# Performance work log

Hardware: AMD Instinct MI355X
Metric: run time of the kernel (lower is better)

Reference implementation:

```python
import jax, jax.numpy as jnp
import numpy as np
import math

# ---- hyperparameters (init_kwargs) ----
D = 2              # spatial dimension
MTOT = 65          # quadrature nodes per dimension (odd)
LENGTHSCALE = 0.1  # SE kernel lengthscale
OUTPUTSCALE = 1.0  # SE kernel variance
SIGMASQ = 0.05     # observation noise variance
CG_ITERS = 30      # fixed CG iteration count (replaces tol-based early stopping)
N_TRAIN = 100000
N_TEST = 50000
TWO_PI = 2.0 * math.pi


def setup_inputs() -> dict:
    key = jax.random.key(0)
    k1, k2, k3 = jax.random.split(key, 3)
    x = jax.random.uniform(k1, (N_TRAIN, D), dtype=jnp.float32)
    y = jax.random.normal(k2, (N_TRAIN,), dtype=jnp.float32)
    x_new = jax.random.uniform(k3, (N_TEST, D), dtype=jnp.float32)
    return {"x": x, "y": y, "x_new": x_new}


def _phases(col, h, freqs, isign):
    # exp(isign * i * 2*pi*h * x * k), shape [N, K]
    return jnp.exp((1j * isign * TWO_PI) * (h * col[:, None] * freqs[None, :]).astype(jnp.float32))


def _nudft_type1(pts, c, h, freqs):
    # fk[a,b] = sum_n c_n exp(-2*pi*i*h*(k_a x_n0 + k_b x_n1)); separable tensor grid
    E0 = _phases(pts[:, 0], h, freqs, -1.0)
    E1 = _phases(pts[:, 1], h, freqs, -1.0)
    return jnp.einsum('n,na,nb->ab', c.astype(jnp.complex64), E0, E1)


def _nudft_type2(pts, fk, h, freqs):
    # f_n = sum_{a,b} fk[a,b] exp(+2*pi*i*h*(k_a x_n0 + k_b x_n1))
    E0 = _phases(pts[:, 0], h, freqs, +1.0)
    E1 = _phases(pts[:, 1], h, freqs, +1.0)
    return jnp.einsum('ab,na,nb->n', fk, E0, E1)


def _cg(A, b, iters):
    # complex Hermitian-PSD conjugate gradients, fixed iteration count
    x0 = jnp.zeros_like(b)
    r0 = b
    rs0 = jnp.real(jnp.vdot(r0, r0))

    def step(carry, _):
        xk, r, p, rs = carry
        Ap = A(p)
        alpha = rs / jnp.real(jnp.vdot(p, Ap))
        xk = xk + alpha * p
        r = r - alpha * Ap
        rs_new = jnp.real(jnp.vdot(r, r))
        p = r + (rs_new / rs) * p
        return (xk, r, p, rs_new), None

    (xk, _, _, _), _ = jax.lax.scan(step, (x0, r0, r0, rs0), None, length=iters)
    return xk


def _forward(x, y, x_new):
    m = (MTOT - 1) // 2
    # geometry / quadrature (get_xis): domain extent L, spacing h = 1/L, grid k = -m..m
    x_all = jnp.concatenate((x, x_new), axis=0)
    L = jnp.max(jnp.max(x_all, axis=0) - jnp.min(x_all, axis=0))
    L = jnp.where(L <= 1e-9, jnp.float32(1.0), L)
    h = (1.0 / L).astype(jnp.float32)
    k = (jnp.arange(MTOT) - m).astype(jnp.float32)
    xis_1d = h * k
    X0, X1 = jnp.meshgrid(xis_1d, xis_1d, indexing='ij')
    sq = X0 * X0 + X1 * X1  # [MTOT, MTOT] squared frequency norm
    # squared-exponential spectral density S(s) = sigma_f^2 (2*pi*l^2)^(d/2) exp(-2*pi^2*l^2 |s|^2)
    l2 = LENGTHSCALE * LENGTHSCALE
    spec = OUTPUTSCALE * (TWO_PI * l2) ** (D / 2) * jnp.exp((-2.0 * math.pi ** 2 * l2) * sq)
    ws = jnp.sqrt(spec * h ** D).reshape(-1).astype(jnp.complex64)  # [M]

    # rhs = ws * F^H y  (type-1 NUFFT, exact NUDFT)
    rhs = ws * _nudft_type1(x, y, h, k).reshape(-1)

    # Toeplitz convolution vector v[o] = sum_n exp(-2*pi*i*h*o.x_n), offsets -(mtot-1)..(mtot-1)
    kk = (jnp.arange(2 * MTOT - 1) - (MTOT - 1)).astype(jnp.float32)
    Ev0 = _phases(x[:, 0], h, kk, -1.0)
    Ev1 = _phases(x[:, 1], h, kk, -1.0)
    v = jnp.einsum('na,nb->ab', Ev0, Ev1)  # [2M-1, 2M-1]
    # circularly align offset 0 to index 0, precompute FFT
    v_circ = jnp.roll(v, shift=(-(MTOT - 1), -(MTOT - 1)), axis=(0, 1))
    vhat = jnp.fft.fftn(v_circ)
    s_fft = (2 * MTOT - 1, 2 * MTOT - 1)

    def toeplitz_apply(w):  # w: [MTOT, MTOT] complex
        W = jnp.fft.fftn(w, s=s_fft)
        full = jnp.fft.ifftn(vhat * W)
        return full[:MTOT, :MTOT]

    def A_mean(beta):  # (W F^H F W + sigma^2 I) beta, beta flat [M]
        wb = (ws * beta).reshape(MTOT, MTOT)
        Tw = toeplitz_apply(wb).reshape(-1)
        return ws * Tw + SIGMASQ * beta

    beta = _cg(A_mean, rhs, CG_ITERS)
    # posterior mean at test points via type-2 NUFFT
    yhat = jnp.real(_nudft_type2(x_new, (ws * beta).reshape(MTOT, MTOT), h, k))
    return yhat


def reference(x, y, x_new):
    return _forward(x, y, x_new)
```

## Files before the change

kernel.cpp:

```cpp
#include <hip/hip_runtime.h>
#include <math.h>

#define M2 4225
#define NTRAIN 100000
#define NTEST 50000
#define CGITERS 30
#define TWO_PI_D 6.283185307179586476925287
#define TPI32 6.28318530717958647692f

#define F_H 0
#define F_RS 1
#define F_PAP 2
#define F_RSN 3
#define F_WS 8
#define F_RHS 4234
#define F_X 12684
#define F_R 21134
#define F_P 29584
#define F_AP 38034
#define F_PB 46484
#define F_VF 50710
#define F_VHAT 83992
#define F_PROD 117274
#define D_VPART 125330
#define D_FKPART 2271890

#define NCHUNK 128
#define PTSB2 782
#define VHALF 8385
#define VH2 16770
#define FKHALF 2145
#define FH2 4290

__device__ __forceinline__ unsigned fkey(float f){
  unsigned u = __float_as_uint(f);
  return (u & 0x80000000u) ? ~u : (u | 0x80000000u);
}
__device__ __forceinline__ float fdec(unsigned k){
  unsigned u = (k & 0x80000000u) ? (k & 0x7fffffffu) : ~k;
  return __uint_as_float(u);
}

__global__ void k_init(unsigned* mm){
  if (threadIdx.x == 0){
    mm[0] = 0xFFFFFFFFu; mm[1] = 0u; mm[2] = 0xFFFFFFFFu; mm[3] = 0u;
  }
}

__global__ void k_minmax(const float* __restrict__ x, const float* __restrict__ xn,
                         unsigned* __restrict__ mm){
  int tid = blockIdx.x * blockDim.x + threadIdx.x;
  int str = gridDim.x * blockDim.x;
  float mn0 = 1e30f, mx0 = -1e30f, mn1 = 1e30f, mx1 = -1e30f;
  const float2* a = (const float2*)x;
  for (int i = tid; i < NTRAIN; i += str){
    float2 v = a[i];
    mn0 = fminf(mn0, v.x); mx0 = fmaxf(mx0, v.x);
    mn1 = fminf(mn1, v.y); mx1 = fmaxf(mx1, v.y);
  }
  const float2* b = (const float2*)xn;
  for (int i = tid; i < NTEST; i += str){
    float2 v = b[i];
    mn0 = fminf(mn0, v.x); mx0 = fmaxf(mx0, v.x);
    mn1 = fminf(mn1, v.y); mx1 = fmaxf(mx1, v.y);
  }
  for (int off = 32; off; off >>= 1){
    mn0 = fminf(mn0, __shfl_xor(mn0, off, 64));
    mx0 = fmaxf(mx0, __shfl_xor(mx0, off, 64));
    mn1 = fminf(mn1, __shfl_xor(mn1, off, 64));
    mx1 = fmaxf(mx1, __shfl_xor(mx1, off, 64));
  }
  if ((threadIdx.x & 63) == 0){
    atomicMin(&mm[0], fkey(mn0)); atomicMax(&mm[1], fkey(mx0));
    atomicMin(&mm[2], fkey(mn1)); atomicMax(&mm[3], fkey(mx1));
  }
}

__global__ void k_setup(float* __restrict__ wsf){
  const unsigned* mm = (const unsigned*)(wsf + 4);
  float mn0 = fdec(mm[0]), mx0 = fdec(mm[1]);
  float mn1 = fdec(mm[2]), mx1 = fdec(mm[3]);
  float d0 = __fsub_rn(mx0, mn0), d1 = __fsub_rn(mx1, mn1);
  float L = fmaxf(d0, d1);
  if (L <= 1e-9f) L = 1.0f;
  float hf = __fdiv_rn(1.0f, L);
  if (threadIdx.x == 0) wsf[F_H] = hf;
  const float c0f = (float)(TWO_PI_D * 0.01);
  const float c1f = (float)(-2.0 * 9.869604401089358618834 * 0.01);
  float h2f = __fmul_rn(hf, hf);
  for (int e = threadIdx.x; e < M2; e += blockDim.x){
    int r = e / 65, c = e - r * 65;
    float xi0 = __fmul_rn(hf, (float)(r - 32));
    float xi1 = __fmul_rn(hf, (float)(c - 32));
    float sq = __fadd_rn(__fmul_rn(xi0, xi0), __fmul_rn(xi1, xi1));
    float spec = __fmul_rn(c0f, expf(__fmul_rn(c1f, sq)));
    wsf[F_WS + e] = sqrtf(__fmul_rn(spec, h2f));
  }
}

__launch_bounds__(256)
__global__ void k_v_main(const float* __restrict__ x, const float* __restrict__ wsf,
                         double* __restrict__ vpart){
  __shared__ float2 aL[16][80];
  __shared__ float2 bL[16][16];
  __shared__ float hxs[16][2];
  const float hf = wsf[F_H];
  const int tid = threadIdx.x;
  const int t0 = tid >> 4, t1 = tid & 15;
  const int jcol = blockIdx.y * 16 + t1;
  double2 acc[5];
  #pragma unroll
  for (int k = 0; k < 5; ++k) acc[k] = make_double2(0.0, 0.0);
  const int p0 = blockIdx.x * PTSB2;
  const int pend = min(p0 + PTSB2, NTRAIN);
  for (int base = p0; base < pend; base += 16){
    if (tid < 32){
      int p = tid >> 1, d = tid & 1;
      int gp = base + p;
      hxs[p][d] = (gp < pend) ? __fmul_rn(hf, x[2 * gp + d]) : 0.f;
    }
    __syncthreads();
    for (int i = tid; i < 16 * 80; i += 256){
      int p = i / 80;
      int o = i - p * 80;
      int gp = base + p;
      float2 va = make_float2(0.f, 0.f);
      if (gp < pend && o < 65){
        float t = __fmul_rn(hxs[p][0], (float)o);
        float sn, cs; sincosf(__fmul_rn(TPI32, t), &sn, &cs);
        va = make_float2(cs, -sn);
      }
      aL[p][o] = va;
    }
    {
      int p = t0, c = t1;
      int gp = base + p;
      int j = blockIdx.y * 16 + c;
      float2 vb = make_float2(0.f, 0.f);
      if (gp < pend && j < 129){
        float t = __fmul_rn(hxs[p][1], (float)(j - 64));
        float sn, cs; sincosf(__fmul_rn(TPI32, t), &sn, &cs);
        vb = make_float2(cs, -sn);
      }
      bL[p][c] = vb;
    }
    __syncthreads();
    #pragma unroll 1
    for (int p = 0; p < 16; ++p){
      float2 bv = bL[p][t1];
      float2 av[5];
      #pragma unroll
      for (int k = 0; k < 5; ++k) av[k] = aL[p][t0 + 16 * k];
      #pragma unroll
      for (int k = 0; k < 5; ++k){
        acc[k].x += (double)av[k].x * (double)bv.x - (double)av[k].y * (double)bv.y;
        acc[k].y += (double)av[k].x * (double)bv.y + (double)av[k].y * (double)bv.x;
      }
    }
    __syncthreads();
  }
  double* outp = vpart + (size_t)blockIdx.x * VH2;
  if (jcol < 129){
    #pragma unroll
    for (int k = 0; k < 5; ++k){
      int o0 = t0 + 16 * k;
      if (o0 < 65){
        int e = o0 * 129 + jcol;
        outp[2 * e] = acc[k].x;
        outp[2 * e + 1] = acc[k].y;
      }
    }
  }
}

__launch_bounds__(256)
__global__ void k_fk_main(const float* __restrict__ x, const float* __restrict__ y,
                          const float* __restrict__ wsf, double* __restrict__ fkpart){
  __shared__ float2 aL[16][48];
  __shared__ float2 bL[16][16];
  __shared__ float hxs[16][2];
  __shared__ float ys[16];
  const float hf = wsf[F_H];
  const int tid = threadIdx.x;
  const int t0 = tid >> 4, t1 = tid & 15;
  const int jcol = blockIdx.y * 16 + t1;
  double2 acc[3];
  #pragma unroll
  for (int k = 0; k < 3; ++k) acc[k] = make_double2(0.0, 0.0);
  const int p0 = blockIdx.x * PTSB2;
  const int pend = min(p0 + PTSB2, NTRAIN);
  for (int base = p0; base < pend; base += 16){
    if (tid < 32){
      int p = tid >> 1, d = tid & 1;
      int gp = base + p;
      hxs[p][d] = (gp < pend) ? __fmul_rn(hf, x[2 * gp + d]) : 0.f;
    } else if (tid < 48){
      int p = tid - 32;
      int gp = base + p;
      ys[p] = (gp < pend) ? y[gp] : 0.f;
    }
    __syncthreads();
    for (int i = tid; i < 16 * 48; i += 256){
      int p = i / 48, o = i - p * 48;
      int gp = base + p;
      float2 val = make_float2(0.f, 0.f);
      if (o < 33 && gp < pend){
        float t = __fmul_rn(hxs[p][0], (float)o);
        float sn, cs; sincosf(__fmul_rn(TPI32, t), &sn, &cs);
        val = make_float2(__fmul_rn(ys[p], cs), __fmul_rn(ys[p], -sn));
      }
      aL[p][o] = val;
    }
    {
      int p = t0, c = t1;
      int gp = base + p;
      int j = blockIdx.y * 16 + c;
      float2 vb = make_float2(0.f, 0.f);
      if (gp < pend && j < 65){
        float t = __fmul_rn(hxs[p][1], (float)(j - 32));
        float sn, cs; sincosf(__fmul_rn(TPI32, t), &sn, &cs);
        vb = make_float2(cs, -sn);
      }
      bL[p][c] = vb;
    }
    __syncthreads();
    #pragma unroll 1
    for (int p = 0; p < 16; ++p){
      float2 bv = bL[p][t1];
      float2 av[3];
      #pragma unroll
      for (int k = 0; k < 3; ++k) av[k] = aL[p][t0 + 16 * k];
      #pragma unroll
      for (int k = 0; k < 3; ++k){
        acc[k].x += (double)av[k].x * (double)bv.x - (double)av[k].y * (double)bv.y;
        acc[k].y += (double)av[k].x * (double)bv.y + (double)av[k].y * (double)bv.x;
      }
    }
    __syncthreads();
  }
  double* outp = fkpart + (size_t)blockIdx.x * FH2;
  if (jcol < 65){
    #pragma unroll
    for (int k = 0; k < 3; ++k){
      int o0 = t0 + 16 * k;
      if (o0 < 33){
        int e = o0 * 65 + jcol;
        outp[2 * e] = acc[k].x;
        outp[2 * e + 1] = acc[k].y;
      }
    }
  }
}

__global__ void k_reduce_v(const double* __restrict__ wsd, float* __restrict__ wsf){
  int e = blockIdx.x * blockDim.x + threadIdx.x;
  if (e >= VHALF) return;
  const double* vp = wsd + D_VPART;
  double sr = 0.0, si = 0.0;
  for (int k = 0; k < NCHUNK; ++k){
    sr += vp[(size_t)k * VH2 + 2 * e];
    si += vp[(size_t)k * VH2 + 2 * e + 1];
  }
  float r32 = (float)sr, i32 = (float)si;
  int o0 = e / 129, j = e - o0 * 129;
  float2* vF = (float2*)(wsf + F_VF);
  vF[(o0 + 64) * 129 + j] = make_float2(r32, i32);
  if (o0 > 0) vF[(64 - o0) * 129 + (128 - j)] = make_float2(r32, -i32);
}

__global__ void k_reduce_fk(const double* __restrict__ wsd, float* __restrict__ wsf){
  int e = blockIdx.x * blockDim.x + threadIdx.x;
  if (e >= FKHALF) return;
  const double* fp = wsd + D_FKPART;
  double sr = 0.0, si = 0.0;
  for (int k = 0; k < NCHUNK; ++k){
    sr += fp[(size_t)k * FH2 + 2 * e];
    si += fp[(size_t)k * FH2 + 2 * e + 1];
  }
  float fr = (float)sr, fi = (float)si;
  int a = e / 65, c = e - a * 65;
  int ef = (a + 32) * 65 + c;
  float wf = wsf[F_WS + ef];
  float* rhs = wsf + F_RHS;
  rhs[2 * ef] = __fmul_rn(wf, fr);
  rhs[2 * ef + 1] = __fmul_rn(wf, fi);
  if (a > 0){
    int ef2 = (32 - a) * 65 + (64 - c);
    float wf2 = wsf[F_WS + ef2];
    rhs[2 * ef2] = __fmul_rn(wf2, fr);
    rhs[2 * ef2 + 1] = -__fmul_rn(wf2, fi);
  }
}

__launch_bounds__(192)
__global__ void k_vhat(float* __restrict__ wsf){
  __shared__ double twc[129], tws[129];
  __shared__ double t1r[129], t1i[129];
  int p = blockIdx.x, t = threadIdx.x;
  if (t < 129){
    double ang = TWO_PI_D * (double)t / 129.0;
    double s, c; sincos(ang, &s, &c);
    twc[t] = c; tws[t] = s;
  }
  __syncthreads();
  if (t < 129){
    const float2* vF = (const float2*)(wsf + F_VF);
    int n = t;
    int nsrc = (n + 64) % 129;
    double ar = 0.0, ai = 0.0;
    for (int m = 0; m < 129; ++m){
      float2 v = vF[((m + 64) % 129) * 129 + nsrc];
      int idx = (p * m) % 129;
      double wr = twc[idx], wi = -tws[idx];
      ar += (double)v.x * wr - (double)v.y * wi;
      ai += (double)v.x * wi + (double)v.y * wr;
    }
    t1r[n] = ar; t1i[n] = ai;
  }
  __syncthreads();
  if (t < 129){
    int q = t;
    double ar = 0.0, ai = 0.0;
    for (int n = 0; n < 129; ++n){
      int idx = (q * n) % 129;
      double wr = twc[idx], wi = -tws[idx];
      ar += t1r[n] * wr - t1i[n] * wi;
      ai += t1r[n] * wi + t1i[n] * wr;
    }
    ((float2*)(wsf + F_VHAT))[p * 129 + q] = make_float2((float)ar, (float)ai);
  }
}

__global__ void k_cg_init(float* __restrict__ wsf){
  int e = blockIdx.x * blockDim.x + threadIdx.x;
  if (e >= M2) return;
  const float2* rhs = (const float2*)(wsf + F_RHS);
  float2 b = rhs[e];
  ((float2*)(wsf + F_X))[e] = make_float2(0.f, 0.f);
  ((float2*)(wsf + F_R))[e] = b;
  ((float2*)(wsf + F_P))[e] = b;
  wsf[F_PB + e] = __fadd_rn(__fmul_rn(b.x, b.x), __fmul_rn(b.y, b.y));
}

__device__ __forceinline__ float pw_leaf(const float* d, int o, int n){
  float r0 = d[o], r1 = d[o+1], r2 = d[o+2], r3 = d[o+3];
  float r4 = d[o+4], r5 = d[o+5], r6 = d[o+6], r7 = d[o+7];
  int i = 8;
  int lim = n - (n & 7);
  for (; i < lim; i += 8){
    r0 = __fadd_rn(r0, d[o+i]);   r1 = __fadd_rn(r1, d[o+i+1]);
    r2 = __fadd_rn(r2, d[o+i+2]); r3 = __fadd_rn(r3, d[o+i+3]);
    r4 = __fadd_rn(r4, d[o+i+4]); r5 = __fadd_rn(r5, d[o+i+5]);
    r6 = __fadd_rn(r6, d[o+i+6]); r7 = __fadd_rn(r7, d[o+i+7]);
  }
  float res = __fadd_rn(__fadd_rn(__fadd_rn(r0, r1), __fadd_rn(r2, r3)),
                        __fadd_rn(__fadd_rn(r4, r5), __fadd_rn(r6, r7)));
  for (; i < n; ++i) res = __fadd_rn(res, d[o+i]);
  return res;
}

__device__ __forceinline__ void pw_tree(const float* pb, float* T, int tid){
  if (tid < 16){
    const int tb[16] = {0,264,528,792,1056,1320,1584,1848,
                        2112,2376,2640,2904,3168,3432,3696,3960};
    int base = tb[tid];
    int sz3 = (tid == 15) ? 73 : 72;
    float L0 = pw_leaf(pb, base, 128);
    float L1 = pw_leaf(pb, base + 128, 64);
    float L2 = pw_leaf(pb, base + 192, sz3);
    T[tid] = __fadd_rn(L0, __fadd_rn(L1, L2));
  }
  __syncthreads();
  if (tid == 0){
    float s0 = __fadd_rn(__fadd_rn(T[0], T[1]), __fadd_rn(T[2], T[3]));
    float s1 = __fadd_rn(__fadd_rn(T[4], T[5]), __fadd_rn(T[6], T[7]));
    float s2 = __fadd_rn(__fadd_rn(T[8], T[9]), __fadd_rn(T[10], T[11]));
    float s3 = __fadd_rn(__fadd_rn(T[12], T[13]), __fadd_rn(T[14], T[15]));
    T[0] = __fadd_rn(__fadd_rn(s0, s1), __fadd_rn(s2, s3));
  }
}

__launch_bounds__(256)
__global__ void k_pair0(float* __restrict__ wsf){
  __shared__ float pb[M2];
  __shared__ float T[16];
  int tid = threadIdx.x;
  for (int i = tid; i < M2; i += 256) pb[i] = wsf[F_PB + i];
  __syncthreads();
  pw_tree(pb, T, tid);
  __syncthreads();
  if (tid == 0) wsf[F_RS] = T[0];
}

__launch_bounds__(192)
__global__ void k_wfft(float* __restrict__ wsf){
  __shared__ double twc[129], tws[129];
  __shared__ double t1r[65], t1i[65];
  int pr = blockIdx.x, t = threadIdx.x;
  if (t < 129){
    double ang = TWO_PI_D * (double)t / 129.0;
    double s, c; sincos(ang, &s, &c);
    twc[t] = c; tws[t] = s;
  }
  __syncthreads();
  if (t < 65){
    const float2* P = (const float2*)(wsf + F_P);
    const float* W = wsf + F_WS;
    int n = t;
    double ar = 0.0, ai = 0.0;
    for (int m = 0; m < 65; ++m){
      int e = m * 65 + n;
      float2 p = P[e];
      float w = W[e];
      float wbr = __fmul_rn(w, p.x), wbi = __fmul_rn(w, p.y);
      int idx = (pr * m) % 129;
      double wr = twc[idx], wi = -tws[idx];
      ar += (double)wbr * wr - (double)wbi * wi;
      ai += (double)wbr * wi + (double)wbi * wr;
    }
    t1r[n] = ar; t1i[n] = ai;
  }
  __syncthreads();
  if (t < 129){
    int q = t;
    double ar = 0.0, ai = 0.0;
    for (int n = 0; n < 65; ++n){
      int idx = (q * n) % 129;
      double wr = twc[idx], wi = -tws[idx];
      ar += t1r[n] * wr - t1i[n] * wi;
      ai += t1r[n] * wi + t1i[n] * wr;
    }
    float Wr = (float)ar, Wi = (float)ai;
    float2 v = ((const float2*)(wsf + F_VHAT))[pr * 129 + q];
    float prre = __fsub_rn(__fmul_rn(v.x, Wr), __fmul_rn(v.y, Wi));
    float prim = __fadd_rn(__fmul_rn(v.x, Wi), __fmul_rn(v.y, Wr));
    ((float2*)(wsf + F_PROD))[pr * 129 + q] = make_float2(prre, prim);
  }
}

__launch_bounds__(192)
__global__ void k_ifft(float* __restrict__ wsf){
  __shared__ double twc[129], tws[129];
  __shared__ double ur[129], ui[129];
  int m = blockIdx.x, t = threadIdx.x;
  if (t < 129){
    double ang = TWO_PI_D * (double)t / 129.0;
    double s, c; sincos(ang, &s, &c);
    twc[t] = c; tws[t] = s;
  }
  __syncthreads();
  if (t < 129){
    const float2* prod = (const float2*)(wsf + F_PROD);
    int q = t;
    double ar = 0.0, ai = 0.0;
    for (int pr = 0; pr < 129; ++pr){
      float2 v = prod[pr * 129 + q];
      int idx = (m * pr) % 129;
      double wr = twc[idx], wi = tws[idx];
      ar += (double)v.x * wr - (double)v.y * wi;
      ai += (double)v.x * wi + (double)v.y * wr;
    }
    const double sc = 1.0 / 129.0;
    ur[q] = ar * sc; ui[q] = ai * sc;
  }
  __syncthreads();
  if (t < 65){
    int n = t;
    double ar = 0.0, ai = 0.0;
    for (int q = 0; q < 129; ++q){
      int idx = (n * q) % 129;
      double wr = twc[idx], wi = tws[idx];
      ar += ur[q] * wr - ui[q] * wi;
      ai += ur[q] * wi + ui[q] * wr;
    }
    const double sc = 1.0 / 129.0;
    float Twr = (float)(ar * sc), Twi = (float)(ai * sc);
    int e = m * 65 + n;
    float w = wsf[F_WS + e];
    float2 p = ((const float2*)(wsf + F_P))[e];
    float Apx = __fadd_rn(__fmul_rn(w, Twr), __fmul_rn(0.05f, p.x));
    float Apy = __fadd_rn(__fmul_rn(w, Twi), __fmul_rn(0.05f, p.y));
    ((float2*)(wsf + F_AP))[e] = make_float2(Apx, Apy);
    wsf[F_PB + e] = __fadd_rn(__fmul_rn(p.x, Apx), __fmul_rn(p.y, Apy));
  }
}

__launch_bounds__(256)
__global__ void k_cgstep(float* __restrict__ wsf){
  __shared__ float pb[M2];
  __shared__ float T[16];
  __shared__ float sh[2];
  int tid = threadIdx.x;
  for (int i = tid; i < M2; i += 256) pb[i] = wsf[F_PB + i];
  __syncthreads();
  pw_tree(pb, T, tid);
  __syncthreads();
  if (tid == 0){
    float rs = wsf[F_RS];
    sh[1] = rs;
    sh[0] = __fdiv_rn(rs, T[0]);
  }
  __syncthreads();
  float alpha = sh[0];
  float2* X = (float2*)(wsf + F_X);
  float2* R = (float2*)(wsf + F_R);
  float2* P = (float2*)(wsf + F_P);
  const float2* AP = (const float2*)(wsf + F_AP);
  for (int e = tid; e < M2; e += 256){
    float2 p = P[e], ap = AP[e], xv = X[e], rv = R[e];
    xv.x = __fadd_rn(xv.x, __fmul_rn(alpha, p.x));
    xv.y = __fadd_rn(xv.y, __fmul_rn(alpha, p.y));
    rv.x = __fsub_rn(rv.x, __fmul_rn(alpha, ap.x));
    rv.y = __fsub_rn(rv.y, __fmul_rn(alpha, ap.y));
    X[e] = xv; R[e] = rv;
    pb[e] = __fadd_rn(__fmul_rn(rv.x, rv.x), __fmul_rn(rv.y, rv.y));
  }
  __syncthreads();
  pw_tree(pb, T, tid);
  __syncthreads();
  if (tid == 0){
    float rsn = T[0];
    sh[0] = __fdiv_rn(rsn, sh[1]);
    wsf[F_RS] = rsn;
  }
  __syncthreads();
  float beta = sh[0];
  for (int e = tid; e < M2; e += 256){
    float2 rv = R[e], p = P[e];
    P[e] = make_float2(__fadd_rn(rv.x, __fmul_rn(beta, p.x)),
                       __fadd_rn(rv.y, __fmul_rn(beta, p.y)));
  }
}

__launch_bounds__(256)
__global__ void k_predict(const float* __restrict__ xn, const float* __restrict__ wsf,
                          float* __restrict__ out){
  __shared__ double fbRe[M2];
  __shared__ double fbIm[M2];
  const float hf = wsf[F_H];
  const float* wsq = wsf + F_WS;
  const float2* xb = (const float2*)(wsf + F_X);
  int tid = threadIdx.x;
  for (int i = tid; i < M2; i += 256){
    float w = wsq[i]; float2 q = xb[i];
    fbRe[i] = (double)__fmul_rn(w, q.x);
    fbIm[i] = (double)__fmul_rn(w, q.y);
  }
  __syncthreads();
  int lane = tid & 63;
  int wid = (blockIdx.x * 256 + tid) >> 6;
  int nw = (gridDim.x * 256) >> 6;
  for (int n = wid; n < NTEST; n += nw){
    float hx0 = __fmul_rn(hf, xn[2 * n]);
    float hx1 = __fmul_rn(hf, xn[2 * n + 1]);
    float t0 = __fmul_rn(hx0, (float)(lane - 32));
    float s0, c0; sincosf(__fmul_rn(TPI32, t0), &s0, &c0);
    float t1 = __fmul_rn(hx1, (float)(lane - 32));
    float s1, c1; sincosf(__fmul_rn(TPI32, t1), &s1, &c1);
    float t0x = __fmul_rn(hx0, 32.0f);
    float s0x, c0x; sincosf(__fmul_rn(TPI32, t0x), &s0x, &c0x);
    float t1x = __fmul_rn(hx1, 32.0f);
    float s1x, c1x; sincosf(__fmul_rn(TPI32, t1x), &s1x, &c1x);
    double e0r = (double)c0, e0i = (double)s0;
    double e1r = (double)c1, e1i = (double)s1;
    double gr = 0.0, gi = 0.0;
    for (int a = 0; a < 64; ++a){
      double er = __shfl(e0r, a, 64);
      double ei = __shfl(e0i, a, 64);
      double fr = fbRe[a * 65 + lane];
      double fi = fbIm[a * 65 + lane];
      gr += fr * er - fi * ei;
      gi += fr * ei + fi * er;
    }
    {
      double fr = fbRe[64 * 65 + lane], fi = fbIm[64 * 65 + lane];
      gr += fr * (double)c0x - fi * (double)s0x;
      gi += fr * (double)s0x + fi * (double)c0x;
    }
    double contrib = gr * e1r - gi * e1i;
    {
      double fr = fbRe[lane * 65 + 64], fi = fbIm[lane * 65 + 64];
      double ur = fr * e0r - fi * e0i;
      double ui = fr * e0i + fi * e0r;
      contrib += ur * (double)c1x - ui * (double)s1x;
      if (lane == 0){
        double fr2 = fbRe[64 * 65 + 64], fi2 = fbIm[64 * 65 + 64];
        double vr = fr2 * (double)c0x - fi2 * (double)s0x;
        double vi = fr2 * (double)s0x + fi2 * (double)c0x;
        contrib += vr * (double)c1x - vi * (double)s1x;
      }
    }
    for (int off = 32; off; off >>= 1) contrib += __shfl_xor(contrib, off, 64);
    if (lane == 0) out[n] = (float)contrib;
  }
}

extern "C" void kernel_launch(void* const* d_in, const int* in_sizes, int n_in,
                              void* d_out, int out_size, void* d_ws, size_t ws_size,
                              hipStream_t stream){
  const float* x = (const float*)d_in[0];
  const float* y = (const float*)d_in[1];
  const float* xnew = (const float*)d_in[2];
  float* wsf = (float*)d_ws;
  double* wsd = (double*)d_ws;
  float* out = (float*)d_out;
  unsigned* mm = (unsigned*)(wsf + 4);

  k_init<<<1, 64, 0, stream>>>(mm);
  k_minmax<<<256, 256, 0, stream>>>(x, xnew, mm);
  k_setup<<<1, 256, 0, stream>>>(wsf);
  k_v_main<<<dim3(NCHUNK, 9), 256, 0, stream>>>(x, wsf, wsd + D_VPART);
  k_fk_main<<<dim3(NCHUNK, 5), 256, 0, stream>>>(x, y, wsf, wsd + D_FKPART);
  k_reduce_v<<<33, 256, 0, stream>>>(wsd, wsf);
  k_reduce_fk<<<9, 256, 0, stream>>>(wsd, wsf);
  k_vhat<<<129, 192, 0, stream>>>(wsf);
  k_cg_init<<<17, 256, 0, stream>>>(wsf);
  k_pair0<<<1, 256, 0, stream>>>(wsf);
  for (int it = 0; it < CGITERS; ++it){
    k_wfft<<<129, 192, 0, stream>>>(wsf);
    k_ifft<<<65, 192, 0, stream>>>(wsf);
    k_cgstep<<<1, 256, 0, stream>>>(wsf);
  }
  k_predict<<<256, 256, 0, stream>>>(xnew, wsf, out);
}
```

Measured before the change: 2.381 ms.

## Fuse CG iterations into one persistent kernel with software grid barriers

Replaces the 90 per-iteration launches (wfft, ifft, cgstep) with a single persistent 129-block kernel that loops over the CG iterations and uses atomic-counter grid barriers between phases. Twiddle index modulo operations are also replaced with incremental add-and-wrap. The goal is to remove kernel launch overhead and twiddle recomputation per iteration. The barrier relies on all 129 blocks being co-resident, and the single-block cgstep phase leaves the other blocks spinning.

```diff
diff --git a/kernel.cpp b/kernel.cpp
--- a/kernel.cpp
+++ b/kernel.cpp
@@ -10,8 +10,8 @@
 
 #define F_H 0
 #define F_RS 1
-#define F_PAP 2
-#define F_RSN 3
+#define F_CNT 2
+#define F_GEN 3
 #define F_WS 8
 #define F_RHS 4234
 #define F_X 12684
@@ -31,6 +31,7 @@
 #define VH2 16770
 #define FKHALF 2145
 #define FH2 4290
+#define NBLK 129u
 
 __device__ __forceinline__ unsigned fkey(float f){
   unsigned u = __float_as_uint(f);
@@ -333,6 +334,10 @@
 
 __global__ void k_cg_init(float* __restrict__ wsf){
   int e = blockIdx.x * blockDim.x + threadIdx.x;
+  if (e == 0){
+    ((unsigned*)wsf)[F_CNT] = 0u;
+    ((unsigned*)wsf)[F_GEN] = 0u;
+  }
   if (e >= M2) return;
   const float2* rhs = (const float2*)(wsf + F_RHS);
   float2 b = rhs[e];
@@ -392,143 +397,164 @@
   if (tid == 0) wsf[F_RS] = T[0];
 }
 
-__launch_bounds__(192)
-__global__ void k_wfft(float* __restrict__ wsf){
+__device__ __forceinline__ void gridbar(unsigned* cnt, unsigned* gen){
+  __syncthreads();
+  if (threadIdx.x == 0){
+    __threadfence();
+    unsigned g = atomicAdd(gen, 0u);
+    unsigned old = atomicAdd(cnt, 1u);
+    if (old == NBLK - 1u){
+      atomicExch(cnt, 0u);
+      __threadfence();
+      atomicAdd(gen, 1u);
+    } else {
+      while (atomicAdd(gen, 0u) == g){ __builtin_amdgcn_s_sleep(4); }
+    }
+    __threadfence();
+  }
+  __syncthreads();
+}
+
+__launch_bounds__(256)
+__global__ void k_cgloop(float* __restrict__ wsf){
   __shared__ double twc[129], tws[129];
-  __shared__ double t1r[65], t1i[65];
-  int pr = blockIdx.x, t = threadIdx.x;
+  __shared__ double d1[129], d2[129];
+  __shared__ float pb[M2];
+  __shared__ float T[16];
+  __shared__ float sh[2];
+  const int bid = blockIdx.x;
+  const int t = threadIdx.x;
+  unsigned* cnt = ((unsigned*)wsf) + F_CNT;
+  unsigned* gen = ((unsigned*)wsf) + F_GEN;
   if (t < 129){
     double ang = TWO_PI_D * (double)t / 129.0;
     double s, c; sincos(ang, &s, &c);
     twc[t] = c; tws[t] = s;
   }
   __syncthreads();
-  if (t < 65){
-    const float2* P = (const float2*)(wsf + F_P);
-    const float* W = wsf + F_WS;
-    int n = t;
-    double ar = 0.0, ai = 0.0;
-    for (int m = 0; m < 65; ++m){
-      int e = m * 65 + n;
-      float2 p = P[e];
-      float w = W[e];
-      float wbr = __fmul_rn(w, p.x), wbi = __fmul_rn(w, p.y);
-      int idx = (pr * m) % 129;
-      double wr = twc[idx], wi = -tws[idx];
-      ar += (double)wbr * wr - (double)wbi * wi;
-      ai += (double)wbr * wi + (double)wbi * wr;
-    }
-    t1r[n] = ar; t1i[n] = ai;
-  }
-  __syncthreads();
-  if (t < 129){
-    int q = t;
-    double ar = 0.0, ai = 0.0;
-    for (int n = 0; n < 65; ++n){
-      int idx = (q * n) % 129;
-      double wr = twc[idx], wi = -tws[idx];
-      ar += t1r[n] * wr - t1i[n] * wi;
-      ai += t1r[n] * wi + t1i[n] * wr;
-    }
-    float Wr = (float)ar, Wi = (float)ai;
-    float2 v = ((const float2*)(wsf + F_VHAT))[pr * 129 + q];
-    float prre = __fsub_rn(__fmul_rn(v.x, Wr), __fmul_rn(v.y, Wi));
-    float prim = __fadd_rn(__fmul_rn(v.x, Wi), __fmul_rn(v.y, Wr));
-    ((float2*)(wsf + F_PROD))[pr * 129 + q] = make_float2(prre, prim);
-  }
-}
-
-__launch_bounds__(192)
-__global__ void k_ifft(float* __restrict__ wsf){
-  __shared__ double twc[129], tws[129];
-  __shared__ double ur[129], ui[129];
-  int m = blockIdx.x, t = threadIdx.x;
-  if (t < 129){
-    double ang = TWO_PI_D * (double)t / 129.0;
-    double s, c; sincos(ang, &s, &c);
-    twc[t] = c; tws[t] = s;
-  }
-  __syncthreads();
-  if (t < 129){
-    const float2* prod = (const float2*)(wsf + F_PROD);
-    int q = t;
-    double ar = 0.0, ai = 0.0;
-    for (int pr = 0; pr < 129; ++pr){
-      float2 v = prod[pr * 129 + q];
-      int idx = (m * pr) % 129;
-      double wr = twc[idx], wi = tws[idx];
-      ar += (double)v.x * wr - (double)v.y * wi;
-      ai += (double)v.x * wi + (double)v.y * wr;
-    }
-    const double sc = 1.0 / 129.0;
-    ur[q] = ar * sc; ui[q] = ai * sc;
-  }
-  __syncthreads();
-  if (t < 65){
-    int n = t;
-    double ar = 0.0, ai = 0.0;
-    for (int q = 0; q < 129; ++q){
-      int idx = (n * q) % 129;
-      double wr = twc[idx], wi = tws[idx];
-      ar += ur[q] * wr - ui[q] * wi;
-      ai += ur[q] * wi + ui[q] * wr;
-    }
-    const double sc = 1.0 / 129.0;
-    float Twr = (float)(ar * sc), Twi = (float)(ai * sc);
-    int e = m * 65 + n;
-    float w = wsf[F_WS + e];
-    float2 p = ((const float2*)(wsf + F_P))[e];
-    float Apx = __fadd_rn(__fmul_rn(w, Twr), __fmul_rn(0.05f, p.x));
-    float Apy = __fadd_rn(__fmul_rn(w, Twi), __fmul_rn(0.05f, p.y));
-    ((float2*)(wsf + F_AP))[e] = make_float2(Apx, Apy);
-    wsf[F_PB + e] = __fadd_rn(__fmul_rn(p.x, Apx), __fmul_rn(p.y, Apy));
-  }
-}
-
-__launch_bounds__(256)
-__global__ void k_cgstep(float* __restrict__ wsf){
-  __shared__ float pb[M2];
-  __shared__ float T[16];
-  __shared__ float sh[2];
-  int tid = threadIdx.x;
-  for (int i = tid; i < M2; i += 256) pb[i] = wsf[F_PB + i];
-  __syncthreads();
-  pw_tree(pb, T, tid);
-  __syncthreads();
-  if (tid == 0){
-    float rs = wsf[F_RS];
-    sh[1] = rs;
-    sh[0] = __fdiv_rn(rs, T[0]);
-  }
-  __syncthreads();
-  float alpha = sh[0];
+  float2* PROD = (float2*)(wsf + F_PROD);
+  const float2* VHAT = (const float2*)(wsf + F_VHAT);
   float2* X = (float2*)(wsf + F_X);
   float2* R = (float2*)(wsf + F_R);
   float2* P = (float2*)(wsf + F_P);
-  const float2* AP = (const float2*)(wsf + F_AP);
-  for (int e = tid; e < M2; e += 256){
-    float2 p = P[e], ap = AP[e], xv = X[e], rv = R[e];
-    xv.x = __fadd_rn(xv.x, __fmul_rn(alpha, p.x));
-    xv.y = __fadd_rn(xv.y, __fmul_rn(alpha, p.y));
-    rv.x = __fsub_rn(rv.x, __fmul_rn(alpha, ap.x));
-    rv.y = __fsub_rn(rv.y, __fmul_rn(alpha, ap.y));
-    X[e] = xv; R[e] = rv;
-    pb[e] = __fadd_rn(__fmul_rn(rv.x, rv.x), __fmul_rn(rv.y, rv.y));
-  }
-  __syncthreads();
-  pw_tree(pb, T, tid);
-  __syncthreads();
-  if (tid == 0){
-    float rsn = T[0];
-    sh[0] = __fdiv_rn(rsn, sh[1]);
-    wsf[F_RS] = rsn;
-  }
-  __syncthreads();
-  float beta = sh[0];
-  for (int e = tid; e < M2; e += 256){
-    float2 rv = R[e], p = P[e];
-    P[e] = make_float2(__fadd_rn(rv.x, __fmul_rn(beta, p.x)),
-                       __fadd_rn(rv.y, __fmul_rn(beta, p.y)));
+  float2* AP = (float2*)(wsf + F_AP);
+  const float* W = wsf + F_WS;
+
+  for (int it = 0; it < CGITERS; ++it){
+    {
+      const int pr = bid;
+      if (t < 65){
+        int n = t;
+        double ar = 0.0, ai = 0.0;
+        int idx = 0;
+        for (int m = 0; m < 65; ++m){
+          int e = m * 65 + n;
+          float2 p = P[e];
+          float w = W[e];
+          float wbr = __fmul_rn(w, p.x), wbi = __fmul_rn(w, p.y);
+          double wr = twc[idx], wi = -tws[idx];
+          ar += (double)wbr * wr - (double)wbi * wi;
+          ai += (double)wbr * wi + (double)wbi * wr;
+          idx += pr; if (idx >= 129) idx -= 129;
+        }
+        d1[n] = ar; d2[n] = ai;
+      }
+      __syncthreads();
+      if (t < 129){
+        int q = t;
+        double ar = 0.0, ai = 0.0;
+        int idx = 0;
+        for (int n = 0; n < 65; ++n){
+          double wr = twc[idx], wi = -tws[idx];
+          ar += d1[n] * wr - d2[n] * wi;
+          ai += d1[n] * wi + d2[n] * wr;
+          idx += q; if (idx >= 129) idx -= 129;
+        }
+        float Wr = (float)ar, Wi = (float)ai;
+        float2 v = VHAT[pr * 129 + q];
+        float prre = __fsub_rn(__fmul_rn(v.x, Wr), __fmul_rn(v.y, Wi));
+        float prim = __fadd_rn(__fmul_rn(v.x, Wi), __fmul_rn(v.y, Wr));
+        PROD[pr * 129 + q] = make_float2(prre, prim);
+      }
+    }
+    gridbar(cnt, gen);
+    if (bid < 65){
+      const int m = bid;
+      if (t < 129){
+        int q = t;
+        double ar = 0.0, ai = 0.0;
+        int idx = 0;
+        for (int pr = 0; pr < 129; ++pr){
+          float2 v = PROD[pr * 129 + q];
+          double wr = twc[idx], wi = tws[idx];
+          ar += (double)v.x * wr - (double)v.y * wi;
+          ai += (double)v.x * wi + (double)v.y * wr;
+          idx += m; if (idx >= 129) idx -= 129;
+        }
+        const double sc = 1.0 / 129.0;
+        d1[q] = ar * sc; d2[q] = ai * sc;
+      }
+      __syncthreads();
+      if (t < 65){
+        int n = t;
+        double ar = 0.0, ai = 0.0;
+        int idx = 0;
+        for (int q = 0; q < 129; ++q){
+          double wr = twc[idx], wi = tws[idx];
+          ar += d1[q] * wr - d2[q] * wi;
+          ai += d1[q] * wi + d2[q] * wr;
+          idx += n; if (idx >= 129) idx -= 129;
+        }
+        const double sc = 1.0 / 129.0;
+        float Twr = (float)(ar * sc), Twi = (float)(ai * sc);
+        int e = m * 65 + n;
+        float w = W[e];
+        float2 p = P[e];
+        float Apx = __fadd_rn(__fmul_rn(w, Twr), __fmul_rn(0.05f, p.x));
+        float Apy = __fadd_rn(__fmul_rn(w, Twi), __fmul_rn(0.05f, p.y));
+        AP[e] = make_float2(Apx, Apy);
+        wsf[F_PB + e] = __fadd_rn(__fmul_rn(p.x, Apx), __fmul_rn(p.y, Apy));
+      }
+    }
+    gridbar(cnt, gen);
+    if (bid == 0){
+      for (int i = t; i < M2; i += 256) pb[i] = wsf[F_PB + i];
+      __syncthreads();
+      pw_tree(pb, T, t);
+      __syncthreads();
+      if (t == 0){
+        float rs = wsf[F_RS];
+        sh[1] = rs;
+        sh[0] = __fdiv_rn(rs, T[0]);
+      }
+      __syncthreads();
+      float alpha = sh[0];
+      for (int e = t; e < M2; e += 256){
+        float2 p = P[e], ap = AP[e], xv = X[e], rv = R[e];
+        xv.x = __fadd_rn(xv.x, __fmul_rn(alpha, p.x));
+        xv.y = __fadd_rn(xv.y, __fmul_rn(alpha, p.y));
+        rv.x = __fsub_rn(rv.x, __fmul_rn(alpha, ap.x));
+        rv.y = __fsub_rn(rv.y, __fmul_rn(alpha, ap.y));
+        X[e] = xv; R[e] = rv;
+        pb[e] = __fadd_rn(__fmul_rn(rv.x, rv.x), __fmul_rn(rv.y, rv.y));
+      }
+      __syncthreads();
+      pw_tree(pb, T, t);
+      __syncthreads();
+      if (t == 0){
+        float rsn = T[0];
+        sh[0] = __fdiv_rn(rsn, sh[1]);
+        wsf[F_RS] = rsn;
+      }
+      __syncthreads();
+      float beta = sh[0];
+      for (int e = t; e < M2; e += 256){
+        float2 rv = R[e], p = P[e];
+        P[e] = make_float2(__fadd_rn(rv.x, __fmul_rn(beta, p.x)),
+                           __fadd_rn(rv.y, __fmul_rn(beta, p.y)));
+      }
+    }
+    gridbar(cnt, gen);
   }
 }
 
@@ -616,10 +642,6 @@
   k_vhat<<<129, 192, 0, stream>>>(wsf);
   k_cg_init<<<17, 256, 0, stream>>>(wsf);
   k_pair0<<<1, 256, 0, stream>>>(wsf);
-  for (int it = 0; it < CGITERS; ++it){
-    k_wfft<<<129, 192, 0, stream>>>(wsf);
-    k_ifft<<<65, 192, 0, stream>>>(wsf);
-    k_cgstep<<<1, 256, 0, stream>>>(wsf);
-  }
+  k_cgloop<<<129, 256, 0, stream>>>(wsf);
   k_predict<<<256, 256, 0, stream>>>(xnew, wsf, out);
 }
```

Measured after the change: 3.123 ms. 31.1% more time.
